# Kernel tuning notes

Hardware: AMD Instinct MI355X
Metric: run time of the kernel (lower is better)

## Reference

```python
import jax, jax.numpy as jnp
import numpy as np
from jax import lax

INPUT_DIM = 512
KERNEL_DIM = 3
HEADS = 8
B, L = 16, 1024


def setup_inputs() -> dict:
    key = jax.random.key(0)
    ks = jax.random.split(key, 4)
    fan = INPUT_DIM * KERNEL_DIM
    std = float(np.sqrt(2.0 / (INPUT_DIM + fan)))  # xavier_normal for conv weight
    x = jax.random.normal(ks[0], (B, INPUT_DIM, L), dtype=jnp.float32)
    w0 = jax.random.normal(ks[1], (INPUT_DIM, INPUT_DIM, KERNEL_DIM), dtype=jnp.float32) * std
    w1 = jax.random.normal(ks[2], (INPUT_DIM, INPUT_DIM, KERNEL_DIM), dtype=jnp.float32) * std
    w2 = jax.random.normal(ks[3], (INPUT_DIM, INPUT_DIM, KERNEL_DIM), dtype=jnp.float32) * std
    b0 = jnp.zeros((INPUT_DIM,), jnp.float32)
    b1 = jnp.zeros((INPUT_DIM,), jnp.float32)
    b2 = jnp.zeros((INPUT_DIM,), jnp.float32)
    return {"x": x, "w0": w0, "b0": b0, "w1": w1, "b1": b1, "w2": w2, "b2": b2}


def _conv1d(x, w, b):
    # x: [B, C, L], w: [O, I, K] -> [B, O, L-K+1] (VALID, stride 1)
    y = lax.conv_general_dilated(x, w, window_strides=(1,), padding='VALID',
                                 dimension_numbers=('NCH', 'OIH', 'NCH'))
    return y + b[None, :, None]


def _multihead_attention(q, k, v, input_dim, heads):
    # q,k,v: [B, D, Lp]; chunk along channel dim == reshape to [B, H, Dh, Lp]
    b, d, lp = q.shape
    dh = d // heads
    qh = q.reshape(b, heads, dh, lp)
    kh = k.reshape(b, heads, dh, lp)
    vh = v.reshape(b, heads, dh, lp)
    scale = 1.0 / np.sqrt(input_dim)  # NOTE: original scales by sqrt(full input_dim)
    scores = jnp.einsum('bhdq,bhdk->bhqk', qh, kh) * scale  # [B,H,Lp,Lp]
    attn = jax.nn.softmax(scores, axis=-1)
    out = jnp.einsum('bhqk,bhdk->bhdq', attn, vh)  # [B,H,Dh,Lp]
    return out.reshape(b, d, lp)


def reference(x, w0, b0, w1, b1, w2, b2):
    q = _conv1d(x, w0, b0)
    k = _conv1d(x, w1, b1)
    v = _conv1d(x, w2, b2)
    return _multihead_attention(q, k, v, INPUT_DIM, HEADS)
```

## Files before the change

kernel.cpp:

```cpp
#include <hip/hip_runtime.h>

#define B_SZ 16
#define CIN  512
#define LIN  1024
#define LP   1022
#define HEADS 8
#define DH    64

typedef __attribute__((ext_vector_type(8))) short bf16x8;
typedef __attribute__((ext_vector_type(4))) float f32x4;

__device__ inline unsigned short f2bf(float f) {
    union { float f; unsigned int u; } c; c.f = f;
    unsigned int r = c.u + 0x7FFF + ((c.u >> 16) & 1);
    return (unsigned short)(r >> 16);
}

__device__ __forceinline__ void gl_lds16(const unsigned short* g, unsigned short* l) {
    __builtin_amdgcn_global_load_lds((const __attribute__((address_space(1))) void*)g,
                                     (__attribute__((address_space(3))) void*)l, 16, 0, 0);
}

#define SWZ(G) ((G) ^ (((G) >> 3) & 7))

__global__ __launch_bounds__(256) void xb_cvt_kernel(const float* __restrict__ x,
                                                     unsigned short* __restrict__ xb) {
    __shared__ float sm[64][68];
    const int t  = threadIdx.x;
    const int l0 = blockIdx.x * 64;
    const int i0 = blockIdx.y * 64;
    const int b  = blockIdx.z;
    const float* S = x + ((size_t)b * CIN + i0) * LIN;

    #pragma unroll
    for (int rr = 0; rr < 4; rr++) {
        int idx = rr * 1024 + t * 4;
        int ii = idx >> 6, lj = idx & 63;
        *(float4*)&sm[ii][lj] = *(const float4*)(S + (size_t)ii * LIN + l0 + lj);
    }
    __syncthreads();

    #pragma unroll
    for (int rr = 0; rr < 4; rr++) {
        int idx = rr * 1024 + t * 4;
        int l = idx >> 6, dj = idx & 63;
        ushort4 h;
        h.x = f2bf(sm[dj + 0][l]);
        h.y = f2bf(sm[dj + 1][l]);
        h.z = f2bf(sm[dj + 2][l]);
        h.w = f2bf(sm[dj + 3][l]);
        *(ushort4*)(xb + ((size_t)b * 1024 + l0 + l) * 512 + i0 + dj) = h;
    }
}

__global__ __launch_bounds__(256) void wb_cvt_kernel(const float* __restrict__ w0,
                                                     const float* __restrict__ w1,
                                                     const float* __restrict__ w2,
                                                     unsigned short* __restrict__ wb) {
    const int kk = blockIdx.y;
    int flat = blockIdx.x * 256 + threadIdx.x;
    int i  = flat & 511;
    int oG = flat >> 9;
    int c  = oG >> 9, o = oG & 511;
    const float* w = (c == 0) ? w0 : (c == 1) ? w1 : w2;
    wb[(size_t)kk * 786432 + flat] = f2bf(w[o * 1536 + i * 3 + kk]);
}

__global__ __launch_bounds__(256) void conv_mfma_kernel(
        const unsigned short* __restrict__ xb,
        const unsigned short* __restrict__ wb,
        const float* __restrict__ b0, const float* __restrict__ b1,
        const float* __restrict__ b2,
        unsigned short* __restrict__ Qt, unsigned short* __restrict__ Kt,
        unsigned short* __restrict__ Vt, float qscale) {
    __shared__ unsigned short smem[16896];
    unsigned short* xs = smem;
    unsigned short* ws = smem + 4224;

    const int t    = threadIdx.x;
    const int wave = t >> 6;
    const int lane = t & 63;
    const int col  = lane & 15;
    const int quad = lane >> 4;
    const int wh   = wave >> 1;
    const int wn   = wave & 1;
    const int l0   = blockIdx.x * 128;
    const int o0   = blockIdx.y * 128;
    const int b    = blockIdx.z;

    f32x4 acc[4][4];
    #pragma unroll
    for (int i = 0; i < 4; i++)
        #pragma unroll
        for (int j = 0; j < 4; j++) acc[i][j] = (f32x4){0.f, 0.f, 0.f, 0.f};

    const unsigned short* xrow = xb + (size_t)b * 1024 * 512;

    for (int ic = 0; ic < 512; ic += 32) {
        __syncthreads();

        #pragma unroll
        for (int j = 0; j < 6; j++) {
            int instr = wave * 6 + j;
            int Gg = SWZ(instr * 64 + lane);
            int p = Gg >> 2, q = Gg & 3;
            int kk = p >> 7, orow = p & 127;
            gl_lds16(wb + ((size_t)(kk * 1536 + o0 + orow)) * 512 + ic + q * 8,
                     ws + instr * 512);
        }
        #pragma unroll
        for (int j = 0; j < 2; j++) {
            int instr = wave * 2 + j;
            int Gg = SWZ(instr * 64 + lane);
            int p = Gg >> 2, q = Gg & 3;
            gl_lds16(xrow + (size_t)(l0 + p) * 512 + ic + q * 8,
                     xs + instr * 512);
        }
        if (t < 8) {
            int row = 128 + (t >> 2), sg = t & 3;
            int gl = l0 + row;
            bf16x8 v = (bf16x8){0, 0, 0, 0, 0, 0, 0, 0};
            if (gl < 1024) v = *(const bf16x8*)(xrow + (size_t)gl * 512 + ic + sg * 8);
            *(bf16x8*)&xs[SWZ(512 + t) * 8] = v;
        }
        __syncthreads();

        #pragma unroll
        for (int kk = 0; kk < 3; kk++) {
            bf16x8 af[4], bfr[4];
            #pragma unroll
            for (int ms = 0; ms < 4; ms++) {
                int G = ((kk * 128 + wh * 64 + ms * 16 + col) << 2) | quad;
                af[ms] = *(const bf16x8*)&ws[SWZ(G) * 8];
            }
            #pragma unroll
            for (int ns = 0; ns < 4; ns++) {
                int G = ((wn * 64 + ns * 16 + col + kk) << 2) | quad;
                bfr[ns] = *(const bf16x8*)&xs[SWZ(G) * 8];
            }
            #pragma unroll
            for (int ms = 0; ms < 4; ms++)
                #pragma unroll
                for (int ns = 0; ns < 4; ns++)
                    acc[ms][ns] = __builtin_amdgcn_mfma_f32_16x16x32_bf16(af[ms], bfr[ns], acc[ms][ns], 0, 0, 0);
        }
    }

    const int c = blockIdx.y >> 2;

    if (c < 2) {
        unsigned short* dst = (c == 0) ? Qt : Kt;
        const float* bias   = (c == 0) ? b0 : b1;
        const float sc      = (c == 0) ? qscale : 1.0f;
        const int h = (((o0 & 511) + wh * 64) >> 6) & 7;
        unsigned short* base = dst + (size_t)(b * 8 + h) * 65536;
        #pragma unroll
        for (int ms = 0; ms < 4; ms++) {
            int ob = (o0 & 511) + wh * 64 + ms * 16 + quad * 4;
            float bv[4];
            #pragma unroll
            for (int r = 0; r < 4; r++) bv[r] = bias[ob + r];
            int d0 = ms * 16 + quad * 4;
            #pragma unroll
            for (int ns = 0; ns < 4; ns++) {
                int l = l0 + wn * 64 + ns * 16 + col;
                ushort4 hv;
                hv.x = f2bf((acc[ms][ns][0] + bv[0]) * sc);
                hv.y = f2bf((acc[ms][ns][1] + bv[1]) * sc);
                hv.z = f2bf((acc[ms][ns][2] + bv[2]) * sc);
                hv.w = f2bf((acc[ms][ns][3] + bv[3]) * sc);
                *(ushort4*)(base + (size_t)l * 64 + d0) = hv;
            }
        }
    } else {
        __syncthreads();
        unsigned short* vt = smem;
        #pragma unroll
        for (int ms = 0; ms < 4; ms++) {
            int ob = (o0 & 511) + wh * 64 + ms * 16 + quad * 4;
            #pragma unroll
            for (int ns = 0; ns < 4; ns++) {
                int lc = wn * 64 + ns * 16 + col;
                #pragma unroll
                for (int r = 0; r < 4; r++)
                    vt[(wh * 64 + ms * 16 + quad * 4 + r) * 132 + lc] =
                        f2bf(acc[ms][ns][r] + b2[ob + r]);
            }
        }
        __syncthreads();
        #pragma unroll
        for (int it = 0; it < 8; it++) {
            int flat = it * 2048 + t * 8;
            int row = flat >> 7, colx = flat & 127;
            bf16x8 v = *(const bf16x8*)&vt[row * 132 + colx];
            int og = (o0 & 511) + row;
            int h = og >> 6, d = og & 63;
            *(bf16x8*)(Vt + ((size_t)(b * 8 + h) * 64 + d) * 1024 + l0 + colx) = v;
        }
    }
}

__global__ __launch_bounds__(256, 2) void attn_kernel(
        const unsigned short* __restrict__ Qt,
        const unsigned short* __restrict__ Kt,
        const unsigned short* __restrict__ Vt,
        float* __restrict__ out) {
    __shared__ unsigned short asmem[34816];
    unsigned short* Ps = asmem + 16384;

    const int t    = threadIdx.x;
    const int wave = t >> 6;
    const int lane = t & 63;
    const int col  = lane & 15;
    const int quad = lane >> 4;

    const int lin = blockIdx.y * 4 + blockIdx.x;
    const int xcd = lin & 7;
    const int idx = lin >> 3;
    const int qb  = idx >> 4;
    const int bh  = xcd * 16 + (idx & 15);

    const size_t base64 = (size_t)bh * 1024 * 64;
    const int q0w = qb * 256 + wave * 64;

    bf16x8 bq[4][2];
    #pragma unroll
    for (int g = 0; g < 4; g++) {
        const unsigned short* qrow = Qt + base64 + (size_t)(q0w + g * 16 + col) * 64;
        bq[g][0] = *(const bf16x8*)(qrow + quad * 8);
        bq[g][1] = *(const bf16x8*)(qrow + 32 + quad * 8);
    }

    const bf16x8 ones = (bf16x8){0x3F80, 0x3F80, 0x3F80, 0x3F80,
                                 0x3F80, 0x3F80, 0x3F80, 0x3F80};

    f32x4 o[4][4];
    #pragma unroll
    for (int g = 0; g < 4; g++)
        #pragma unroll
        for (int d = 0; d < 4; d++) o[g][d] = (f32x4){0.f, 0.f, 0.f, 0.f};
    f32x4 osum[4];
    #pragma unroll
    for (int g = 0; g < 4; g++) osum[g] = (f32x4){0.f, 0.f, 0.f, 0.f};

    const unsigned short* kg0 = Kt + base64;
    const unsigned short* vg  = Vt + base64;
    unsigned short* Pw = Ps + wave * 64 * 72;

    #pragma unroll
    for (int j = 0; j < 2; j++) {
        int i = wave + j * 4;
        int G = SWZ(i * 64 + lane);
        gl_lds16(kg0 + (size_t)G * 8, asmem + i * 512);
        int p = G >> 3, q = G & 7;
        gl_lds16(vg + (size_t)p * 1024 + q * 8, asmem + 4096 + i * 512);
    }
    asm volatile("s_waitcnt vmcnt(0)" ::: "memory");
    __builtin_amdgcn_s_barrier();
    asm volatile("" ::: "memory");

    int cur = 0;
    for (int kt = 0; kt < 16; kt++) {
        if (kt < 15) {
            const unsigned short* kg = kg0 + (size_t)(kt + 1) * 4096;
            unsigned short* Kb = asmem + (cur ^ 1) * 8192;
            #pragma unroll
            for (int j = 0; j < 2; j++) {
                int i = wave + j * 4;
                int G = SWZ(i * 64 + lane);
                gl_lds16(kg + (size_t)G * 8, Kb + i * 512);
                int p = G >> 3, q = G & 7;
                gl_lds16(vg + (size_t)p * 1024 + (kt + 1) * 64 + q * 8,
                         Kb + 4096 + i * 512);
            }
        }

        const unsigned short* Ksb = asmem + cur * 8192;
        const unsigned short* Vsb = Ksb + 4096;

        bf16x8 ak[4][2];
        #pragma unroll
        for (int sub = 0; sub < 4; sub++) {
            int rk = sub * 16 + col;
            ak[sub][0] = *(const bf16x8*)&Ksb[SWZ(rk * 8 + quad) * 8];
            ak[sub][1] = *(const bf16x8*)&Ksb[SWZ(rk * 8 + 4 + quad) * 8];
        }

        #pragma unroll
        for (int g = 0; g < 4; g++) {
            #pragma unroll
            for (int sub = 0; sub < 4; sub++) {
                f32x4 a = (f32x4){0.f, 0.f, 0.f, 0.f};
                __builtin_amdgcn_s_setprio(1);
                a = __builtin_amdgcn_mfma_f32_16x16x32_bf16(ak[sub][0], bq[g][0], a, 0, 0, 0);
                a = __builtin_amdgcn_mfma_f32_16x16x32_bf16(ak[sub][1], bq[g][1], a, 0, 0, 0);
                __builtin_amdgcn_s_setprio(0);
                float e0 = exp2f(a[0]), e1 = exp2f(a[1]);
                float e2 = exp2f(a[2]), e3 = exp2f(a[3]);
                uint2 pk;
                asm("v_cvt_pk_bf16_f32 %0, %1, %2" : "=v"(pk.x) : "v"(e0), "v"(e1));
                asm("v_cvt_pk_bf16_f32 %0, %1, %2" : "=v"(pk.y) : "v"(e2), "v"(e3));
                if (kt == 15 && sub == 3 && quad == 3)
                    pk.y = 0;
                *(uint2*)&Pw[(g * 16 + col) * 72 + sub * 16 + quad * 4] = pk;
            }
        }

        bf16x8 av[4][2];
        #pragma unroll
        for (int dsub = 0; dsub < 4; dsub++) {
            int rd = dsub * 16 + col;
            av[dsub][0] = *(const bf16x8*)&Vsb[SWZ(rd * 8 + quad) * 8];
            av[dsub][1] = *(const bf16x8*)&Vsb[SWZ(rd * 8 + 4 + quad) * 8];
        }

        #pragma unroll
        for (int g = 0; g < 4; g++) {
            bf16x8 bp0 = *(const bf16x8*)&Pw[(g * 16 + col) * 72 + quad * 8];
            bf16x8 bp1 = *(const bf16x8*)&Pw[(g * 16 + col) * 72 + 32 + quad * 8];
            __builtin_amdgcn_s_setprio(1);
            #pragma unroll
            for (int dsub = 0; dsub < 4; dsub++) {
                o[g][dsub] = __builtin_amdgcn_mfma_f32_16x16x32_bf16(av[dsub][0], bp0, o[g][dsub], 0, 0, 0);
                o[g][dsub] = __builtin_amdgcn_mfma_f32_16x16x32_bf16(av[dsub][1], bp1, o[g][dsub], 0, 0, 0);
            }
            osum[g] = __builtin_amdgcn_mfma_f32_16x16x32_bf16(ones, bp0, osum[g], 0, 0, 0);
            osum[g] = __builtin_amdgcn_mfma_f32_16x16x32_bf16(ones, bp1, osum[g], 0, 0, 0);
            __builtin_amdgcn_s_setprio(0);
        }

        asm volatile("s_waitcnt vmcnt(0)" ::: "memory");
        __builtin_amdgcn_s_barrier();
        asm volatile("" ::: "memory");
        cur ^= 1;
    }

    #pragma unroll
    for (int g = 0; g < 4; g++) {
        int q = q0w + g * 16 + col;
        if (q < LP) {
            float inv = 1.0f / osum[g][0];
            #pragma unroll
            for (int dsub = 0; dsub < 4; dsub++) {
                #pragma unroll
                for (int r = 0; r < 4; r++) {
                    int d = dsub * 16 + quad * 4 + r;
                    out[((size_t)bh * 64 + d) * LP + q] = o[g][dsub][r] * inv;
                }
            }
        }
    }
}

extern "C" void kernel_launch(void* const* d_in, const int* in_sizes, int n_in,
                              void* d_out, int out_size, void* d_ws, size_t ws_size,
                              hipStream_t stream) {
    const float* x  = (const float*)d_in[0];
    const float* w0 = (const float*)d_in[1];
    const float* b0 = (const float*)d_in[2];
    const float* w1 = (const float*)d_in[3];
    const float* b1 = (const float*)d_in[4];
    const float* w2 = (const float*)d_in[5];
    const float* b2 = (const float*)d_in[6];
    float* out = (float*)d_out;

    unsigned short* xbp = (unsigned short*)d_ws;
    unsigned short* wbp = xbp + 8388608;
    unsigned short* Qt  = wbp + 2359296;
    unsigned short* Kt  = Qt + 8388608;
    unsigned short* Vt  = Kt + 8388608;

    const float scale = 0.06375870864f;

    xb_cvt_kernel<<<dim3(16, 8, 16), 256, 0, stream>>>(x, xbp);
    wb_cvt_kernel<<<dim3(3072, 3), 256, 0, stream>>>(w0, w1, w2, wbp);
    conv_mfma_kernel<<<dim3(8, 12, 16), 256, 0, stream>>>(xbp, wbp, b0, b1, b2,
                                                          Qt, Kt, Vt, scale);
    attn_kernel<<<dim3(4, 128), 256, 0, stream>>>(Qt, Kt, Vt, out);
}
```

Measured before the change: 239.4 us.

## Rewrite attention with 32x32x16 MFMA keeping probabilities in registers

The attention kernel moves from 16x16x32 to 32x32x16 bf16 MFMA tiles. The probability matrix is repacked across lanes with xor-32 shuffles so it can feed the PV MFMA straight from registers, which removes the per-wave LDS staging buffer for P. The row sums become a scalar accumulation instead of extra MFMAs against a ones vector. Each block now covers 128 queries instead of 256 and the grid doubles, with launch bounds raised to 3 blocks per CU because LDS use shrinks. The costs are shuffle and select overhead, less Q reuse per block, and more redundant K/V loads from global memory.

```diff
diff --git a/kernel.cpp b/kernel.cpp
--- a/kernel.cpp
+++ b/kernel.cpp
@@ -9,6 +9,7 @@
 
 typedef __attribute__((ext_vector_type(8))) short bf16x8;
 typedef __attribute__((ext_vector_type(4))) float f32x4;
+typedef __attribute__((ext_vector_type(16))) float f32x16;
 
 __device__ inline unsigned short f2bf(float f) {
     union { float f; unsigned int u; } c; c.f = f;
@@ -200,52 +201,42 @@
     }
 }
 
-__global__ __launch_bounds__(256, 2) void attn_kernel(
+__global__ __launch_bounds__(256, 3) void attn_kernel(
         const unsigned short* __restrict__ Qt,
         const unsigned short* __restrict__ Kt,
         const unsigned short* __restrict__ Vt,
         float* __restrict__ out) {
-    __shared__ unsigned short asmem[34816];
-    unsigned short* Ps = asmem + 16384;
+    __shared__ unsigned short asmem[16384];
 
     const int t    = threadIdx.x;
     const int wave = t >> 6;
     const int lane = t & 63;
-    const int col  = lane & 15;
-    const int quad = lane >> 4;
-
-    const int lin = blockIdx.y * 4 + blockIdx.x;
+    const int col5 = lane & 31;
+    const int hi   = lane >> 5;
+
+    const int lin = blockIdx.y * 8 + blockIdx.x;
     const int xcd = lin & 7;
     const int idx = lin >> 3;
     const int qb  = idx >> 4;
     const int bh  = xcd * 16 + (idx & 15);
 
-    const size_t base64 = (size_t)bh * 1024 * 64;
-    const int q0w = qb * 256 + wave * 64;
-
-    bf16x8 bq[4][2];
-    #pragma unroll
-    for (int g = 0; g < 4; g++) {
-        const unsigned short* qrow = Qt + base64 + (size_t)(q0w + g * 16 + col) * 64;
-        bq[g][0] = *(const bf16x8*)(qrow + quad * 8);
-        bq[g][1] = *(const bf16x8*)(qrow + 32 + quad * 8);
-    }
-
-    const bf16x8 ones = (bf16x8){0x3F80, 0x3F80, 0x3F80, 0x3F80,
-                                 0x3F80, 0x3F80, 0x3F80, 0x3F80};
-
-    f32x4 o[4][4];
-    #pragma unroll
-    for (int g = 0; g < 4; g++)
-        #pragma unroll
-        for (int d = 0; d < 4; d++) o[g][d] = (f32x4){0.f, 0.f, 0.f, 0.f};
-    f32x4 osum[4];
-    #pragma unroll
-    for (int g = 0; g < 4; g++) osum[g] = (f32x4){0.f, 0.f, 0.f, 0.f};
+    const size_t base64 = (size_t)bh * 65536;
+    const int q0 = qb * 128 + wave * 32;
+
+    bf16x8 bq[4];
+    {
+        const unsigned short* qrow = Qt + base64 + (size_t)(q0 + col5) * 64 + hi * 8;
+        #pragma unroll
+        for (int s = 0; s < 4; s++) bq[s] = *(const bf16x8*)(qrow + s * 16);
+    }
+
+    f32x16 o0, o1;
+    #pragma unroll
+    for (int i = 0; i < 16; i++) { o0[i] = 0.f; o1[i] = 0.f; }
+    float osum = 0.f;
 
     const unsigned short* kg0 = Kt + base64;
     const unsigned short* vg  = Vt + base64;
-    unsigned short* Pw = Ps + wave * 64 * 72;
 
     #pragma unroll
     for (int j = 0; j < 2; j++) {
@@ -278,54 +269,61 @@
         const unsigned short* Ksb = asmem + cur * 8192;
         const unsigned short* Vsb = Ksb + 4096;
 
-        bf16x8 ak[4][2];
-        #pragma unroll
-        for (int sub = 0; sub < 4; sub++) {
-            int rk = sub * 16 + col;
-            ak[sub][0] = *(const bf16x8*)&Ksb[SWZ(rk * 8 + quad) * 8];
-            ak[sub][1] = *(const bf16x8*)&Ksb[SWZ(rk * 8 + 4 + quad) * 8];
-        }
-
-        #pragma unroll
-        for (int g = 0; g < 4; g++) {
-            #pragma unroll
-            for (int sub = 0; sub < 4; sub++) {
-                f32x4 a = (f32x4){0.f, 0.f, 0.f, 0.f};
-                __builtin_amdgcn_s_setprio(1);
-                a = __builtin_amdgcn_mfma_f32_16x16x32_bf16(ak[sub][0], bq[g][0], a, 0, 0, 0);
-                a = __builtin_amdgcn_mfma_f32_16x16x32_bf16(ak[sub][1], bq[g][1], a, 0, 0, 0);
-                __builtin_amdgcn_s_setprio(0);
-                float e0 = exp2f(a[0]), e1 = exp2f(a[1]);
-                float e2 = exp2f(a[2]), e3 = exp2f(a[3]);
-                uint2 pk;
-                asm("v_cvt_pk_bf16_f32 %0, %1, %2" : "=v"(pk.x) : "v"(e0), "v"(e1));
-                asm("v_cvt_pk_bf16_f32 %0, %1, %2" : "=v"(pk.y) : "v"(e2), "v"(e3));
-                if (kt == 15 && sub == 3 && quad == 3)
-                    pk.y = 0;
-                *(uint2*)&Pw[(g * 16 + col) * 72 + sub * 16 + quad * 4] = pk;
-            }
-        }
-
-        bf16x8 av[4][2];
-        #pragma unroll
-        for (int dsub = 0; dsub < 4; dsub++) {
-            int rd = dsub * 16 + col;
-            av[dsub][0] = *(const bf16x8*)&Vsb[SWZ(rd * 8 + quad) * 8];
-            av[dsub][1] = *(const bf16x8*)&Vsb[SWZ(rd * 8 + 4 + quad) * 8];
-        }
-
-        #pragma unroll
-        for (int g = 0; g < 4; g++) {
-            bf16x8 bp0 = *(const bf16x8*)&Pw[(g * 16 + col) * 72 + quad * 8];
-            bf16x8 bp1 = *(const bf16x8*)&Pw[(g * 16 + col) * 72 + 32 + quad * 8];
+        #pragma unroll
+        for (int kb = 0; kb < 2; kb++) {
+            bf16x8 ak[4];
+            #pragma unroll
+            for (int s = 0; s < 4; s++)
+                ak[s] = *(const bf16x8*)&Ksb[SWZ((kb * 32 + col5) * 8 + s * 2 + hi) * 8];
+            bf16x8 av[2][2];
+            #pragma unroll
+            for (int db = 0; db < 2; db++)
+                #pragma unroll
+                for (int s = 0; s < 2; s++)
+                    av[db][s] = *(const bf16x8*)&Vsb[SWZ((db * 32 + col5) * 8 + kb * 4 + s * 2 + hi) * 8];
+
+            f32x16 p;
+            #pragma unroll
+            for (int i = 0; i < 16; i++) p[i] = 0.f;
             __builtin_amdgcn_s_setprio(1);
             #pragma unroll
-            for (int dsub = 0; dsub < 4; dsub++) {
-                o[g][dsub] = __builtin_amdgcn_mfma_f32_16x16x32_bf16(av[dsub][0], bp0, o[g][dsub], 0, 0, 0);
-                o[g][dsub] = __builtin_amdgcn_mfma_f32_16x16x32_bf16(av[dsub][1], bp1, o[g][dsub], 0, 0, 0);
-            }
-            osum[g] = __builtin_amdgcn_mfma_f32_16x16x32_bf16(ones, bp0, osum[g], 0, 0, 0);
-            osum[g] = __builtin_amdgcn_mfma_f32_16x16x32_bf16(ones, bp1, osum[g], 0, 0, 0);
+            for (int s = 0; s < 4; s++)
+                p = __builtin_amdgcn_mfma_f32_32x32x16_bf16(ak[s], bq[s], p, 0, 0, 0);
+            __builtin_amdgcn_s_setprio(0);
+
+            float e[16];
+            #pragma unroll
+            for (int r = 0; r < 16; r++) e[r] = exp2f(p[r]);
+            if (kt == 15 && kb == 1 && hi == 1) { e[14] = 0.f; e[15] = 0.f; }
+            #pragma unroll
+            for (int r = 0; r < 16; r++) osum += e[r];
+
+            bf16x8 bp[2];
+            #pragma unroll
+            for (int s = 0; s < 2; s++) {
+                unsigned int a, b_, c, d;
+                asm("v_cvt_pk_bf16_f32 %0, %1, %2" : "=v"(a)  : "v"(e[s*8+0]), "v"(e[s*8+1]));
+                asm("v_cvt_pk_bf16_f32 %0, %1, %2" : "=v"(b_) : "v"(e[s*8+2]), "v"(e[s*8+3]));
+                asm("v_cvt_pk_bf16_f32 %0, %1, %2" : "=v"(c)  : "v"(e[s*8+4]), "v"(e[s*8+5]));
+                asm("v_cvt_pk_bf16_f32 %0, %1, %2" : "=v"(d)  : "v"(e[s*8+6]), "v"(e[s*8+7]));
+                unsigned int as = (unsigned int)__shfl_xor((int)a,  32);
+                unsigned int bs = (unsigned int)__shfl_xor((int)b_, 32);
+                unsigned int cs = (unsigned int)__shfl_xor((int)c,  32);
+                unsigned int ds = (unsigned int)__shfl_xor((int)d,  32);
+                union { unsigned int u[4]; bf16x8 v; } pk;
+                pk.u[0] = hi ? cs : a;
+                pk.u[1] = hi ? ds : b_;
+                pk.u[2] = hi ? c  : as;
+                pk.u[3] = hi ? d  : bs;
+                bp[s] = pk.v;
+            }
+
+            __builtin_amdgcn_s_setprio(1);
+            #pragma unroll
+            for (int s = 0; s < 2; s++) {
+                o0 = __builtin_amdgcn_mfma_f32_32x32x16_bf16(av[0][s], bp[s], o0, 0, 0, 0);
+                o1 = __builtin_amdgcn_mfma_f32_32x32x16_bf16(av[1][s], bp[s], o1, 0, 0, 0);
+            }
             __builtin_amdgcn_s_setprio(0);
         }
 
@@ -335,19 +333,15 @@
         cur ^= 1;
     }
 
-    #pragma unroll
-    for (int g = 0; g < 4; g++) {
-        int q = q0w + g * 16 + col;
-        if (q < LP) {
-            float inv = 1.0f / osum[g][0];
-            #pragma unroll
-            for (int dsub = 0; dsub < 4; dsub++) {
-                #pragma unroll
-                for (int r = 0; r < 4; r++) {
-                    int d = dsub * 16 + quad * 4 + r;
-                    out[((size_t)bh * 64 + d) * LP + q] = o[g][dsub][r] * inv;
-                }
-            }
+    float osum_t = osum + __shfl_xor(osum, 32);
+    float inv = 1.0f / osum_t;
+    int q = q0 + col5;
+    if (q < LP) {
+        #pragma unroll
+        for (int r = 0; r < 16; r++) {
+            int d0 = (r & 3) + 8 * (r >> 2) + 4 * hi;
+            out[((size_t)(bh * 64 + d0)) * LP + q]      = o0[r] * inv;
+            out[((size_t)(bh * 64 + d0 + 32)) * LP + q] = o1[r] * inv;
         }
     }
 }
@@ -376,5 +370,5 @@
     wb_cvt_kernel<<<dim3(3072, 3), 256, 0, stream>>>(w0, w1, w2, wbp);
     conv_mfma_kernel<<<dim3(8, 12, 16), 256, 0, stream>>>(xbp, wbp, b0, b1, b2,
                                                           Qt, Kt, Vt, scale);
-    attn_kernel<<<dim3(4, 128), 256, 0, stream>>>(Qt, Kt, Vt, out);
-}
+    attn_kernel<<<dim3(8, 128), 256, 0, stream>>>(Qt, Kt, Vt, out);
+}
```

Result: faster. 233.4 us (-2.5%).
